# Kernel optimization log

Hardware: AMD Instinct MI355X
Metric: run time of the kernel (lower is better)

The kernel has to match this reference:

```python
import jax, jax.numpy as jnp
import numpy as np

NCE_T = 0.07   # opt.nce_T
EPS = 1e-8     # torch CosineSimilarity eps
DIAG_FILL = -10.0

N, D = 8192, 256

def setup_inputs() -> dict:
    key = jax.random.key(0)
    kq, kk = jax.random.split(key)
    feat_q = jax.random.normal(kq, (N, D), dtype=jnp.float32)
    feat_k = jax.random.normal(kk, (N, D), dtype=jnp.float32)
    return {"feat_q": feat_q, "feat_k": feat_k}

def reference(feat_q, feat_k):
    # feat_k is detached in the original
    feat_k = jax.lax.stop_gradient(feat_k)
    nq = jnp.linalg.norm(feat_q, axis=-1)            # [N]
    nk = jnp.linalg.norm(feat_k, axis=-1)            # [N]
    # positive cosine similarity (paired rows)
    l_pos = jnp.sum(feat_q * feat_k, axis=-1) / jnp.maximum(nq * nk, EPS)  # [N]
    # full N x N cosine similarity via GEMM (torch does a broadcasted version)
    sim = (feat_q @ feat_k.T) / jnp.maximum(nq[:, None] * nk[None, :], EPS)  # [N,N]
    # mask self-similarities with -10.0 BEFORE dividing by temperature
    diag = jnp.eye(sim.shape[0], dtype=bool)
    l_neg = jnp.where(diag, DIAG_FILL, sim)
    out = jnp.concatenate([l_pos[:, None], l_neg], axis=1) / NCE_T  # [N, N+1]
    # cross-entropy vs target class 0, reduction='none'
    loss = jax.scipy.special.logsumexp(out, axis=1) - out[:, 0]     # [N]
    return loss
```

## Files before the change

### kernel.cpp

```cpp
#include <hip/hip_runtime.h>
#include <stdint.h>
#include <math.h>

#define NROWS 8192
#define DDIM  256
#define BM    128
#define BN    128
#define GJ    16
#define COLS_PER_GROUP (NROWS / GJ)

constexpr float INV_T  = 1.0f / 0.07f;
constexpr float LOG2E  = 1.44269504f;
constexpr float K1     = INV_T * LOG2E;

typedef __bf16 bf16x8 __attribute__((ext_vector_type(8)));
typedef float  f32x4  __attribute__((ext_vector_type(4)));

__device__ __forceinline__ void async_copy16(const uint16_t* g, uint16_t* l) {
    __builtin_amdgcn_global_load_lds(
        (const __attribute__((address_space(1))) uint32_t*)g,
        (__attribute__((address_space(3))) uint32_t*)l, 16, 0, 0);
}

__device__ inline uint16_t f2bf(float f) {
    uint32_t u = __float_as_uint(f);
    u += 0x7fffu + ((u >> 16) & 1u);
    return (uint16_t)(u >> 16);
}

__global__ __launch_bounds__(256) void norm_lpos_kernel(
    const float* __restrict__ fq, const float* __restrict__ fk,
    uint16_t* __restrict__ qb, uint16_t* __restrict__ kb,
    float* __restrict__ lpT)
{
    const int wave = threadIdx.x >> 6;
    const int lane = threadIdx.x & 63;
    const int row  = blockIdx.x * 4 + wave;

    float4 vq = ((const float4*)(fq + (size_t)row * DDIM))[lane];
    float4 vk = ((const float4*)(fk + (size_t)row * DDIM))[lane];
    float sq = vq.x*vq.x + vq.y*vq.y + vq.z*vq.z + vq.w*vq.w;
    float sk = vk.x*vk.x + vk.y*vk.y + vk.z*vk.z + vk.w*vk.w;
    float dp = vq.x*vk.x + vq.y*vk.y + vq.z*vk.z + vq.w*vk.w;
    #pragma unroll
    for (int m = 1; m < 64; m <<= 1) {
        sq += __shfl_xor(sq, m, 64);
        sk += __shfl_xor(sk, m, 64);
        dp += __shfl_xor(dp, m, 64);
    }
    float rq = rsqrtf(sq), rk = rsqrtf(sk);

    ushort4 oq, ok;
    oq.x = f2bf(vq.x * rq); oq.y = f2bf(vq.y * rq); oq.z = f2bf(vq.z * rq); oq.w = f2bf(vq.w * rq);
    ok.x = f2bf(vk.x * rk); ok.y = f2bf(vk.y * rk); ok.z = f2bf(vk.z * rk); ok.w = f2bf(vk.w * rk);
    ((ushort4*)(qb + (size_t)row * DDIM))[lane] = oq;
    ((ushort4*)(kb + (size_t)row * DDIM))[lane] = ok;
    if (lane == 0) lpT[row] = dp * rq * rk * INV_T;
}

__global__ __launch_bounds__(256) void nce_main_kernel(
    const uint16_t* __restrict__ qb, const uint16_t* __restrict__ kb,
    float* __restrict__ gpl)
{
    __shared__ __align__(16) uint16_t lds[2][2][128 * 32];

    const int tid    = threadIdx.x;
    const int wave   = tid >> 6;
    const int lane   = tid & 63;
    const int quad   = lane >> 4;
    const int lanelo = lane & 15;
    const int wr     = wave >> 1;
    const int wc     = wave & 1;
    const int rowBase      = blockIdx.x * BM;
    const int colGroupBase = blockIdx.y * COLS_PER_GROUP;

    const uint16_t* qsrc[2];
    const uint16_t* ksrc[2];
    int dstoff[2];
    #pragma unroll
    for (int i = 0; i < 2; ++i) {
        int S   = i * 256 + tid;
        int row = S >> 2, cp = S & 3;
        int cg  = ((cp + (row >> 2)) & 3) ^ (row & 3);
        qsrc[i] = qb + (size_t)(rowBase + row) * DDIM + cg * 8;
        ksrc[i] = kb + (size_t)(colGroupBase + row) * DDIM + cg * 8;
        dstoff[i] = (i * 256 + wave * 64) * 8;
    }

    int avoff[4], bvoff[4];
    #pragma unroll
    for (int t = 0; t < 4; ++t) {
        int ra = wr * 64 + t * 16 + lanelo;
        avoff[t] = ra * 32 + ((((quad ^ (ra & 3)) - (ra >> 2)) & 3) * 8);
        int rb = wc * 64 + t * 16 + lanelo;
        bvoff[t] = rb * 32 + ((((quad ^ (rb & 3)) - (rb >> 2)) & 3) * 8);
    }

    #pragma unroll
    for (int i = 0; i < 2; ++i) {
        async_copy16(qsrc[i], &lds[0][0][0] + dstoff[i]);
        async_copy16(ksrc[i], &lds[0][1][0] + dstoff[i]);
    }
    __syncthreads();

    float l_run[16];
    #pragma unroll
    for (int i = 0; i < 16; ++i) l_run[i] = 0.f;

    for (int jt = 0; jt < COLS_PER_GROUP / BN; ++jt) {
        f32x4 acc[4][4];
        #pragma unroll
        for (int mt = 0; mt < 4; ++mt)
            #pragma unroll
            for (int nt = 0; nt < 4; ++nt)
                acc[mt][nt] = (f32x4){0.f, 0.f, 0.f, 0.f};

        #pragma unroll
        for (int kk = 0; kk < 8; ++kk) {
            const int p   = jt * 8 + kk;
            const int buf = p & 1;

            if (p < 31) {
                const int np = p + 1;
                const int qo = (np & 7) << 5;
                const int ko = ((np >> 3) << 15) + ((np & 7) << 5);
                #pragma unroll
                for (int i = 0; i < 2; ++i) {
                    async_copy16(qsrc[i] + qo, &lds[buf ^ 1][0][0] + dstoff[i]);
                    async_copy16(ksrc[i] + ko, &lds[buf ^ 1][1][0] + dstoff[i]);
                }
            }

            bf16x8 av[4], bv[4];
            #pragma unroll
            for (int mt = 0; mt < 4; ++mt)
                av[mt] = *(const bf16x8*)&lds[buf][0][avoff[mt]];
            #pragma unroll
            for (int nt = 0; nt < 4; ++nt)
                bv[nt] = *(const bf16x8*)&lds[buf][1][bvoff[nt]];
            #pragma unroll
            for (int mt = 0; mt < 4; ++mt)
                #pragma unroll
                for (int nt = 0; nt < 4; ++nt)
                    acc[mt][nt] = __builtin_amdgcn_mfma_f32_16x16x32_bf16(av[mt], bv[nt], acc[mt][nt], 0, 0, 0);

            __syncthreads();
        }

        #pragma unroll
        for (int mt = 0; mt < 4; ++mt)
            #pragma unroll
            for (int rg = 0; rg < 4; ++rg) {
                float s = 0.f;
                #pragma unroll
                for (int nt = 0; nt < 4; ++nt)
                    s += exp2f(fmaf(acc[mt][nt][rg], K1, -K1));
                l_run[mt * 4 + rg] += s;
            }
    }

    #pragma unroll
    for (int i = 0; i < 16; ++i) {
        float v = l_run[i];
        v += __shfl_xor(v, 1, 64);
        v += __shfl_xor(v, 2, 64);
        v += __shfl_xor(v, 4, 64);
        v += __shfl_xor(v, 8, 64);
        l_run[i] = v;
    }
    float* pl = (float*)&lds[0][0][0];
    if (lanelo == 0) {
        #pragma unroll
        for (int mt = 0; mt < 4; ++mt)
            #pragma unroll
            for (int rg = 0; rg < 4; ++rg) {
                int lr = wr * 64 + mt * 16 + quad * 4 + rg;
                pl[wc * 128 + lr] = l_run[mt * 4 + rg];
            }
    }
    __syncthreads();
    if (tid < 128) {
        float L = pl[tid] + pl[128 + tid];
        gpl[(size_t)blockIdx.y * NROWS + rowBase + tid] = L;
    }
}

__global__ __launch_bounds__(256) void finalize_kernel(
    const float* __restrict__ gpl, const float* __restrict__ lpT,
    float* __restrict__ out)
{
    int t = blockIdx.x * 256 + threadIdx.x;
    if (t >= NROWS) return;
    float L = 0.f;
    #pragma unroll
    for (int g = 0; g < GJ; ++g) L += gpl[g * NROWS + t];
    out[t] = INV_T + __logf(L) - lpT[t];
}

extern "C" void kernel_launch(void* const* d_in, const int* in_sizes, int n_in,
                              void* d_out, int out_size, void* d_ws, size_t ws_size,
                              hipStream_t stream) {
    const float* fq = (const float*)d_in[0];
    const float* fk = (const float*)d_in[1];
    char* ws = (char*)d_ws;
    uint16_t* qb  = (uint16_t*)(ws);
    uint16_t* kb  = (uint16_t*)(ws + 4194304);
    float*    lpT = (float*)(ws + 8388608);
    float*    gpl = (float*)(ws + 8421376);

    norm_lpos_kernel<<<NROWS / 4, 256, 0, stream>>>(fq, fk, qb, kb, lpT);
    dim3 grid(NROWS / BM, GJ);
    nce_main_kernel<<<grid, 256, 0, stream>>>(qb, kb, gpl);
    finalize_kernel<<<NROWS / 256, 256, 0, stream>>>(gpl, lpT, (float*)d_out);
}
```

Measured before the change: 114.8 us.

## Fuse finalize into main kernel via atomic row sums and rotate column-tile order

Removes the separate finalize kernel. Each block atomically adds its per-row partial sums into a zeroed row buffer, and the last block to finish for a row tile (detected with an agent-scope counter) writes the log-loss. The zeroing of the buffer and counters moves into the norm kernel. Column tiles inside each block are visited in a rotated order so concurrent blocks read different K slices at the same time. This saves one launch and a pass over memory, at the cost of atomics and possible order-dependent float summation.

```diff
diff --git a/kernel.cpp b/kernel.cpp
--- a/kernel.cpp
+++ b/kernel.cpp
@@ -31,11 +31,14 @@
 __global__ __launch_bounds__(256) void norm_lpos_kernel(
     const float* __restrict__ fq, const float* __restrict__ fk,
     uint16_t* __restrict__ qb, uint16_t* __restrict__ kb,
-    float* __restrict__ lpT)
+    float* __restrict__ lpT, float* __restrict__ gpl, int* __restrict__ cnt)
 {
     const int wave = threadIdx.x >> 6;
     const int lane = threadIdx.x & 63;
     const int row  = blockIdx.x * 4 + wave;
+
+    if (blockIdx.x < 32) gpl[blockIdx.x * 256 + threadIdx.x] = 0.f;
+    if (blockIdx.x == 32 && threadIdx.x < 64) cnt[threadIdx.x] = 0;
 
     float4 vq = ((const float4*)(fq + (size_t)row * DDIM))[lane];
     float4 vk = ((const float4*)(fk + (size_t)row * DDIM))[lane];
@@ -60,9 +63,11 @@
 
 __global__ __launch_bounds__(256) void nce_main_kernel(
     const uint16_t* __restrict__ qb, const uint16_t* __restrict__ kb,
-    float* __restrict__ gpl)
+    const float* __restrict__ lpT, float* __restrict__ gpl,
+    int* __restrict__ cnt, float* __restrict__ out)
 {
     __shared__ __align__(16) uint16_t lds[2][2][128 * 32];
+    __shared__ int sflag;
 
     const int tid    = threadIdx.x;
     const int wave   = tid >> 6;
@@ -73,6 +78,7 @@
     const int wc     = wave & 1;
     const int rowBase      = blockIdx.x * BM;
     const int colGroupBase = blockIdx.y * COLS_PER_GROUP;
+    const int rot          = (blockIdx.x + blockIdx.y) & 3;
 
     const uint16_t* qsrc[2];
     const uint16_t* ksrc[2];
@@ -99,7 +105,7 @@
     #pragma unroll
     for (int i = 0; i < 2; ++i) {
         async_copy16(qsrc[i], &lds[0][0][0] + dstoff[i]);
-        async_copy16(ksrc[i], &lds[0][1][0] + dstoff[i]);
+        async_copy16(ksrc[i] + (rot << 15), &lds[0][1][0] + dstoff[i]);
     }
     __syncthreads();
 
@@ -123,7 +129,7 @@
             if (p < 31) {
                 const int np = p + 1;
                 const int qo = (np & 7) << 5;
-                const int ko = ((np >> 3) << 15) + ((np & 7) << 5);
+                const int ko = ((((np >> 3) + rot) & 3) << 15) + ((np & 7) << 5);
                 #pragma unroll
                 for (int i = 0; i < 2; ++i) {
                     async_copy16(qsrc[i] + qo, &lds[buf ^ 1][0][0] + dstoff[i]);
@@ -179,22 +185,21 @@
             }
     }
     __syncthreads();
+
     if (tid < 128) {
         float L = pl[tid] + pl[128 + tid];
-        gpl[(size_t)blockIdx.y * NROWS + rowBase + tid] = L;
-    }
-}
-
-__global__ __launch_bounds__(256) void finalize_kernel(
-    const float* __restrict__ gpl, const float* __restrict__ lpT,
-    float* __restrict__ out)
-{
-    int t = blockIdx.x * 256 + threadIdx.x;
-    if (t >= NROWS) return;
-    float L = 0.f;
-    #pragma unroll
-    for (int g = 0; g < GJ; ++g) L += gpl[g * NROWS + t];
-    out[t] = INV_T + __logf(L) - lpT[t];
+        atomicAdd(&gpl[rowBase + tid], L);
+    }
+    __syncthreads();
+    if (tid == 0)
+        sflag = __hip_atomic_fetch_add(&cnt[blockIdx.x], 1,
+                                       __ATOMIC_ACQ_REL, __HIP_MEMORY_SCOPE_AGENT);
+    __syncthreads();
+    if (sflag == GJ - 1 && tid < 128) {
+        int row = rowBase + tid;
+        float L = __hip_atomic_load(&gpl[row], __ATOMIC_RELAXED, __HIP_MEMORY_SCOPE_AGENT);
+        out[row] = INV_T + __logf(L) - lpT[row];
+    }
 }
 
 extern "C" void kernel_launch(void* const* d_in, const int* in_sizes, int n_in,
@@ -207,9 +212,9 @@
     uint16_t* kb  = (uint16_t*)(ws + 4194304);
     float*    lpT = (float*)(ws + 8388608);
     float*    gpl = (float*)(ws + 8421376);
-
-    norm_lpos_kernel<<<NROWS / 4, 256, 0, stream>>>(fq, fk, qb, kb, lpT);
+    int*      cnt = (int*)(ws + 8454144);
+
+    norm_lpos_kernel<<<NROWS / 4, 256, 0, stream>>>(fq, fk, qb, kb, lpT, gpl, cnt);
     dim3 grid(NROWS / BM, GJ);
-    nce_main_kernel<<<grid, 256, 0, stream>>>(qb, kb, gpl);
-    finalize_kernel<<<NROWS / 256, 256, 0, stream>>>(gpl, lpT, (float*)d_out);
-}
+    nce_main_kernel<<<grid, 256, 0, stream>>>(qb, kb, lpT, gpl, cnt, (float*)d_out);
+}
```

Result: slower. 129.5 us (+12.8%).

## Replace LDS-staged column sweep with per-tile direct-load GEMM and atomic row sums

Applied to the files above, without the earlier changes.

The main kernel no longer stages tiles through LDS with async copies and barriers. It launches one block per 128x128 output tile (a 64x64 grid), loads MFMA operands straight from global memory into registers with a 3-deep register prefetch, and adds each row's exp-sum to a global accumulator with atomicAdd. The accumulator is zeroed inside the norm kernel, and finalize reads a single value instead of summing 16 partials. This removes the LDS traffic and syncs, but each block now re-reads its operands from global memory or L2, sends far more atomics, and adds launch overhead for 4096 small blocks. Occupancy is pinned to 2 waves per EU.

```diff
diff --git a/kernel.cpp b/kernel.cpp
--- a/kernel.cpp
+++ b/kernel.cpp
@@ -4,23 +4,13 @@
 
 #define NROWS 8192
 #define DDIM  256
-#define BM    128
-#define BN    128
-#define GJ    16
-#define COLS_PER_GROUP (NROWS / GJ)
 
-constexpr float INV_T  = 1.0f / 0.07f;
-constexpr float LOG2E  = 1.44269504f;
-constexpr float K1     = INV_T * LOG2E;
+constexpr float INV_T = 1.0f / 0.07f;
+constexpr float LOG2E = 1.44269504f;
+constexpr float K1    = INV_T * LOG2E;
 
 typedef __bf16 bf16x8 __attribute__((ext_vector_type(8)));
 typedef float  f32x4  __attribute__((ext_vector_type(4)));
-
-__device__ __forceinline__ void async_copy16(const uint16_t* g, uint16_t* l) {
-    __builtin_amdgcn_global_load_lds(
-        (const __attribute__((address_space(1))) uint32_t*)g,
-        (__attribute__((address_space(3))) uint32_t*)l, 16, 0, 0);
-}
 
 __device__ inline uint16_t f2bf(float f) {
     uint32_t u = __float_as_uint(f);
@@ -31,11 +21,13 @@
 __global__ __launch_bounds__(256) void norm_lpos_kernel(
     const float* __restrict__ fq, const float* __restrict__ fk,
     uint16_t* __restrict__ qb, uint16_t* __restrict__ kb,
-    float* __restrict__ lpT)
+    float* __restrict__ lpT, float* __restrict__ gpl)
 {
     const int wave = threadIdx.x >> 6;
     const int lane = threadIdx.x & 63;
     const int row  = blockIdx.x * 4 + wave;
+
+    if (blockIdx.x < 32) gpl[blockIdx.x * 256 + threadIdx.x] = 0.f;
 
     float4 vq = ((const float4*)(fq + (size_t)row * DDIM))[lane];
     float4 vk = ((const float4*)(fk + (size_t)row * DDIM))[lane];
@@ -58,12 +50,12 @@
     if (lane == 0) lpT[row] = dp * rq * rk * INV_T;
 }
 
-__global__ __launch_bounds__(256) void nce_main_kernel(
+__global__ __launch_bounds__(256)
+__attribute__((amdgpu_waves_per_eu(2, 2)))
+void nce_main_kernel(
     const uint16_t* __restrict__ qb, const uint16_t* __restrict__ kb,
     float* __restrict__ gpl)
 {
-    __shared__ __align__(16) uint16_t lds[2][2][128 * 32];
-
     const int tid    = threadIdx.x;
     const int wave   = tid >> 6;
     const int lane   = tid & 63;
@@ -71,117 +63,67 @@
     const int lanelo = lane & 15;
     const int wr     = wave >> 1;
     const int wc     = wave & 1;
-    const int rowBase      = blockIdx.x * BM;
-    const int colGroupBase = blockIdx.y * COLS_PER_GROUP;
+    const int rowBase = blockIdx.x * 128;
+    const int colBase = blockIdx.y * 128;
 
-    const uint16_t* qsrc[2];
-    const uint16_t* ksrc[2];
-    int dstoff[2];
+    const uint16_t* ap[4];
+    const uint16_t* bp[4];
     #pragma unroll
-    for (int i = 0; i < 2; ++i) {
-        int S   = i * 256 + tid;
-        int row = S >> 2, cp = S & 3;
-        int cg  = ((cp + (row >> 2)) & 3) ^ (row & 3);
-        qsrc[i] = qb + (size_t)(rowBase + row) * DDIM + cg * 8;
-        ksrc[i] = kb + (size_t)(colGroupBase + row) * DDIM + cg * 8;
-        dstoff[i] = (i * 256 + wave * 64) * 8;
+    for (int t = 0; t < 4; ++t) {
+        ap[t] = qb + (size_t)(rowBase + wr * 64 + t * 16 + lanelo) * DDIM + quad * 8;
+        bp[t] = kb + (size_t)(colBase + wc * 64 + t * 16 + lanelo) * DDIM + quad * 8;
     }
 
-    int avoff[4], bvoff[4];
+    bf16x8 af[3][4], bv[3][4];
     #pragma unroll
     for (int t = 0; t < 4; ++t) {
-        int ra = wr * 64 + t * 16 + lanelo;
-        avoff[t] = ra * 32 + ((((quad ^ (ra & 3)) - (ra >> 2)) & 3) * 8);
-        int rb = wc * 64 + t * 16 + lanelo;
-        bvoff[t] = rb * 32 + ((((quad ^ (rb & 3)) - (rb >> 2)) & 3) * 8);
+        af[0][t] = *(const bf16x8*)(ap[t]);
+        bv[0][t] = *(const bf16x8*)(bp[t]);
+        af[1][t] = *(const bf16x8*)(ap[t] + 32);
+        bv[1][t] = *(const bf16x8*)(bp[t] + 32);
     }
 
+    f32x4 acc[4][4];
     #pragma unroll
-    for (int i = 0; i < 2; ++i) {
-        async_copy16(qsrc[i], &lds[0][0][0] + dstoff[i]);
-        async_copy16(ksrc[i], &lds[0][1][0] + dstoff[i]);
-    }
-    __syncthreads();
+    for (int mt = 0; mt < 4; ++mt)
+        #pragma unroll
+        for (int nt = 0; nt < 4; ++nt)
+            acc[mt][nt] = (f32x4){0.f, 0.f, 0.f, 0.f};
 
-    float l_run[16];
     #pragma unroll
-    for (int i = 0; i < 16; ++i) l_run[i] = 0.f;
-
-    for (int jt = 0; jt < COLS_PER_GROUP / BN; ++jt) {
-        f32x4 acc[4][4];
+    for (int kk = 0; kk < 8; ++kk) {
+        const int cur = kk % 3;
+        if (kk < 6) {
+            const int nxt = (kk + 2) % 3;
+            #pragma unroll
+            for (int t = 0; t < 4; ++t) {
+                af[nxt][t] = *(const bf16x8*)(ap[t] + (kk + 2) * 32);
+                bv[nxt][t] = *(const bf16x8*)(bp[t] + (kk + 2) * 32);
+            }
+        }
         #pragma unroll
         for (int mt = 0; mt < 4; ++mt)
             #pragma unroll
             for (int nt = 0; nt < 4; ++nt)
-                acc[mt][nt] = (f32x4){0.f, 0.f, 0.f, 0.f};
-
-        #pragma unroll
-        for (int kk = 0; kk < 8; ++kk) {
-            const int p   = jt * 8 + kk;
-            const int buf = p & 1;
-
-            if (p < 31) {
-                const int np = p + 1;
-                const int qo = (np & 7) << 5;
-                const int ko = ((np >> 3) << 15) + ((np & 7) << 5);
-                #pragma unroll
-                for (int i = 0; i < 2; ++i) {
-                    async_copy16(qsrc[i] + qo, &lds[buf ^ 1][0][0] + dstoff[i]);
-                    async_copy16(ksrc[i] + ko, &lds[buf ^ 1][1][0] + dstoff[i]);
-                }
-            }
-
-            bf16x8 av[4], bv[4];
-            #pragma unroll
-            for (int mt = 0; mt < 4; ++mt)
-                av[mt] = *(const bf16x8*)&lds[buf][0][avoff[mt]];
-            #pragma unroll
-            for (int nt = 0; nt < 4; ++nt)
-                bv[nt] = *(const bf16x8*)&lds[buf][1][bvoff[nt]];
-            #pragma unroll
-            for (int mt = 0; mt < 4; ++mt)
-                #pragma unroll
-                for (int nt = 0; nt < 4; ++nt)
-                    acc[mt][nt] = __builtin_amdgcn_mfma_f32_16x16x32_bf16(av[mt], bv[nt], acc[mt][nt], 0, 0, 0);
-
-            __syncthreads();
-        }
-
-        #pragma unroll
-        for (int mt = 0; mt < 4; ++mt)
-            #pragma unroll
-            for (int rg = 0; rg < 4; ++rg) {
-                float s = 0.f;
-                #pragma unroll
-                for (int nt = 0; nt < 4; ++nt)
-                    s += exp2f(fmaf(acc[mt][nt][rg], K1, -K1));
-                l_run[mt * 4 + rg] += s;
-            }
+                acc[mt][nt] = __builtin_amdgcn_mfma_f32_16x16x32_bf16(
+                    af[cur][mt], bv[cur][nt], acc[mt][nt], 0, 0, 0);
     }
 
     #pragma unroll
-    for (int i = 0; i < 16; ++i) {
-        float v = l_run[i];
-        v += __shfl_xor(v, 1, 64);
-        v += __shfl_xor(v, 2, 64);
-        v += __shfl_xor(v, 4, 64);
-        v += __shfl_xor(v, 8, 64);
-        l_run[i] = v;
-    }
-    float* pl = (float*)&lds[0][0][0];
-    if (lanelo == 0) {
+    for (int mt = 0; mt < 4; ++mt) {
         #pragma unroll
-        for (int mt = 0; mt < 4; ++mt)
+        for (int rg = 0; rg < 4; ++rg) {
+            float s = 0.f;
             #pragma unroll
-            for (int rg = 0; rg < 4; ++rg) {
-                int lr = wr * 64 + mt * 16 + quad * 4 + rg;
-                pl[wc * 128 + lr] = l_run[mt * 4 + rg];
-            }
-    }
-    __syncthreads();
-    if (tid < 128) {
-        float L = pl[tid] + pl[128 + tid];
-        gpl[(size_t)blockIdx.y * NROWS + rowBase + tid] = L;
+            for (int nt = 0; nt < 4; ++nt)
+                s += exp2f(fmaf(acc[mt][nt][rg], K1, -K1));
+            s += __shfl_xor(s, 1, 64);
+            s += __shfl_xor(s, 2, 64);
+            s += __shfl_xor(s, 4, 64);
+            s += __shfl_xor(s, 8, 64);
+            if (lanelo == 0)
+                atomicAdd(&gpl[rowBase + wr * 64 + mt * 16 + quad * 4 + rg], s);
+        }
     }
 }
 
@@ -191,10 +133,7 @@
 {
     int t = blockIdx.x * 256 + threadIdx.x;
     if (t >= NROWS) return;
-    float L = 0.f;
-    #pragma unroll
-    for (int g = 0; g < GJ; ++g) L += gpl[g * NROWS + t];
-    out[t] = INV_T + __logf(L) - lpT[t];
+    out[t] = INV_T + __logf(gpl[t]) - lpT[t];
 }
 
 extern "C" void kernel_launch(void* const* d_in, const int* in_sizes, int n_in,
@@ -208,8 +147,8 @@
     float*    lpT = (float*)(ws + 8388608);
     float*    gpl = (float*)(ws + 8421376);
 
-    norm_lpos_kernel<<<NROWS / 4, 256, 0, stream>>>(fq, fk, qb, kb, lpT);
-    dim3 grid(NROWS / BM, GJ);
+    norm_lpos_kernel<<<NROWS / 4, 256, 0, stream>>>(fq, fk, qb, kb, lpT, gpl);
+    dim3 grid(NROWS / 128, NROWS / 128);
     nce_main_kernel<<<grid, 256, 0, stream>>>(qb, kb, gpl);
     finalize_kernel<<<NROWS / 256, 256, 0, stream>>>(gpl, lpT, (float*)d_out);
 }
```

After: 209.8 us. +82.7%, slower.
